# Kernel tuning notes

Hardware: AMD Instinct MI355X
Metric: run time of the kernel (lower is better)

## Reference

```python
import jax, jax.numpy as jnp
import numpy as np

N_VARS = 2048
D_GRAPH = 256
NUM_ADJ = 7
ALPHA = 0.9
MASK = 0.5


def setup_inputs() -> dict:
    key = jax.random.key(0)
    ks = jax.random.split(key, 8)
    init_adj = jax.random.uniform(ks[0], (N_VARS, N_VARS), dtype=jnp.float32, minval=-1.0, maxval=1.0)
    emb1 = jax.random.normal(ks[1], (NUM_ADJ, N_VARS, D_GRAPH), dtype=jnp.float32)
    emb2 = jax.random.normal(ks[2], (NUM_ADJ, N_VARS, D_GRAPH), dtype=jnp.float32)
    lim = 1.0 / np.sqrt(D_GRAPH)
    w1 = jax.random.uniform(ks[3], (NUM_ADJ, D_GRAPH, D_GRAPH), dtype=jnp.float32, minval=-lim, maxval=lim)
    b1 = jax.random.uniform(ks[4], (NUM_ADJ, D_GRAPH), dtype=jnp.float32, minval=-lim, maxval=lim)
    w2 = jax.random.uniform(ks[5], (NUM_ADJ, D_GRAPH, D_GRAPH), dtype=jnp.float32, minval=-lim, maxval=lim)
    b2 = jax.random.uniform(ks[6], (NUM_ADJ, D_GRAPH), dtype=jnp.float32, minval=-lim, maxval=lim)
    time_indices = jax.random.randint(ks[7], (8,), 0, NUM_ADJ)
    return {
        'init_adj': init_adj, 'emb1': emb1, 'emb2': emb2,
        'w1': w1, 'b1': b1, 'w2': w2, 'b2': b2,
        'time_indices': time_indices, 'current_epoch': 10,
    }


def reference(init_adj, emb1, emb2, w1, b1, w2, b2, time_indices, current_epoch):
    n = init_adj.shape[0]
    k = int(n * n * MASK)
    prop = min(current_epoch / 5, ALPHA)  # static python scalar schedule
    eye = jnp.eye(n, dtype=init_adj.dtype)

    def build_one(e1, e2, W1, B1, W2, B2):
        # nn.Linear: x @ W.T + b, then tanh
        nv1 = jnp.tanh(e1 @ W1.T + B1)          # [n, d]
        nv2 = jnp.tanh(e2 @ W2.T + B2)          # [n, d]
        a = (1.0 - prop) * init_adj + prop * (nv1 @ nv2.T)  # [n, n]
        adj = jax.nn.relu(jnp.tanh(a))
        adj = adj * (1.0 - eye)                 # remove diagonal
        flat = adj.reshape(-1)
        _, idx = jax.lax.top_k(flat, k)         # data-dependent sparsification
        m = jnp.zeros_like(flat).at[idx].set(1.0)
        adj = m.reshape(n, n) * adj
        adj = adj + eye
        return adj / adj.sum(axis=1, keepdims=True)  # row-degree normalize

    oadj = jax.vmap(build_one)(emb1, emb2, w1, b1, w2, b2)  # [num_adj, n, n]
    return oadj[time_indices]  # [B, n, n]
```

## Files before the change

kernel.cpp:

```cpp
#include <hip/hip_runtime.h>
#include <cstdint>
#include <cstddef>

#define NVARS 2048
#define DG    256
#define NSLOT 8
#define NN2   (NVARS*NVARS)
#define K_SEL 2097152u
#define CAP   (1u<<18)
#define KS    512

typedef __attribute__((ext_vector_type(8))) short short8;
typedef __attribute__((ext_vector_type(8))) unsigned short ushort8;
typedef __attribute__((ext_vector_type(4))) float floatx4;

__device__ __align__(16) unsigned short g_ebig[NSLOT][2][NVARS*KS];
__device__ __align__(16) unsigned short g_wbig[NSLOT][2][DG*KS];
__device__ __align__(16) unsigned short g_abig[NSLOT][NVARS*KS];
__device__ __align__(16) unsigned short g_bbig[NSLOT][NVARS*KS];
__device__ unsigned g_hist[NSLOT][2048];
__device__ unsigned g_cand[NSLOT][CAP];
__device__ unsigned g_state[NSLOT][16];
__device__ float g_scal[2];

__device__ __forceinline__ unsigned fkey(float x){
  unsigned b = __float_as_uint(x);
  return (b & 0x80000000u) ? ~b : (b | 0x80000000u);
}
__device__ __forceinline__ unsigned short f2bf(float v){
  unsigned u = __float_as_uint(v);
  return (unsigned short)((u + 0x7FFFu + ((u >> 16) & 1u)) >> 16);
}
__device__ __forceinline__ void async16(void* lds, const void* g){
  __builtin_amdgcn_global_load_lds(
      (const __attribute__((address_space(1))) unsigned int*)g,
      (__attribute__((address_space(3))) unsigned int*)lds, 16, 0, 0);
}

__global__ __launch_bounds__(256) void k_prep(const int* __restrict__ tind,
                                              const int* __restrict__ epoch_p){
  int tid = threadIdx.x;
  if (tid < NSLOT){
    int t = tind[tid];
    int fo = tid;
    for (int b = 0; b < tid; b++){ if (tind[b] == t){ fo = b; break; } }
    g_state[tid][0] = (fo == tid) ? 1u : 0u;
    g_state[tid][1] = (unsigned)fo;
    g_state[tid][2] = 0u;
    g_state[tid][3] = K_SEL;
    g_state[tid][4] = 0u;
    g_state[tid][7] = 0x7FFFFFFFu;
    g_state[tid][8] = 0u;
  }
  if (tid == 0){
    double pd = (double)epoch_p[0] / 5.0;
    if (pd > 0.9) pd = 0.9;
    g_scal[0] = (float)(1.0 - pd);
    g_scal[1] = (float)pd;
  }
  unsigned* h = (unsigned*)g_hist;
  for (int i = tid; i < NSLOT*2048; i += 256) h[i] = 0u;
}

__global__ __launch_bounds__(256) void k_split(
    const float* __restrict__ emb1, const float* __restrict__ emb2,
    const float* __restrict__ w1,  const float* __restrict__ w2,
    const int* __restrict__ tind){
  int z = blockIdx.z; int s = z >> 1; int side = z & 1;
  if (!g_state[s][0]) return;
  int t = tind[s];
  int flat = blockIdx.x*256 + threadIdx.x;
  const float* src;
  unsigned short* dst;
  if (flat < 65536){
    int row = flat >> 5, g8 = flat & 31;
    src = (side ? emb2 : emb1) + (size_t)t*NVARS*DG + (size_t)row*DG + g8*8;
    dst = g_ebig[s][side] + (size_t)row*KS + g8*8;
  } else {
    int f2 = flat - 65536;
    int row = f2 >> 5, g8 = f2 & 31;
    src = (side ? w2 : w1) + (size_t)t*DG*DG + (size_t)row*DG + g8*8;
    dst = g_wbig[s][side] + (size_t)row*KS + g8*8;
  }
  float4 v0 = *(const float4*)src;
  float4 v1 = *(const float4*)(src + 4);
  float a[8] = {v0.x,v0.y,v0.z,v0.w,v1.x,v1.y,v1.z,v1.w};
  ushort8 hi8, lo8;
  #pragma unroll
  for (int j = 0; j < 8; j++){
    unsigned short hb = f2bf(a[j]);
    float hv = __uint_as_float(((unsigned)hb) << 16);
    hi8[j] = hb;
    lo8[j] = f2bf(a[j] - hv);
  }
  *(ushort8*)dst         = hi8;
  *(ushort8*)(dst + 256) = lo8;
}

__global__ __launch_bounds__(256, 2) void k_gemm_nv(
    const float* __restrict__ b1, const float* __restrict__ b2,
    const int* __restrict__ tind){
  int z = blockIdx.z; int s = z >> 1; int side = z & 1;
  if (!g_state[s][0]) return;
  int t = tind[s];
  const unsigned short* __restrict__ A = g_ebig[s][side];
  const unsigned short* __restrict__ B = g_wbig[s][side];
  const float* __restrict__ bias = (side ? b2 : b1) + (size_t)t*DG;
  unsigned short* __restrict__ dst = side ? g_bbig[s] : g_abig[s];
  __shared__ __align__(16) unsigned short As[128*64];
  __shared__ __align__(16) unsigned short Bs[128*64];
  __shared__ __align__(16) float Cs[128][68];
  int tid = threadIdx.x;
  int lane = tid & 63, wv = tid >> 6;
  int rowBase = blockIdx.y*128, colBase = blockIdx.x*128;
  int rW = (wv >> 1)*64, cW = (wv & 1)*64;
  int m = lane & 15, q = lane >> 4;
  int rl = lane >> 3, sl = lane & 7;
  floatx4 acc[4][4] = {};
  for (int p = 0; p < 3; p++){
    int aoff = (p == 1) ? 256 : 0;
    int boff = (p == 2) ? 256 : 0;
    for (int k0 = 0; k0 < 256; k0 += 64){
      #pragma unroll
      for (int t4 = 0; t4 < 4; t4++){
        int rloc = wv*32 + t4*8 + rl;
        int g = sl ^ (rloc & 7);
        async16(&As[(wv*32 + t4*8)*64], A + (size_t)(rowBase + rloc)*KS + aoff + k0 + g*8);
        async16(&Bs[(wv*32 + t4*8)*64], B + (size_t)(colBase + rloc)*KS + boff + k0 + g*8);
      }
      __syncthreads();
      #pragma unroll
      for (int kk = 0; kk < 2; kk++){
        short8 af[4], bfr[4];
        #pragma unroll
        for (int i = 0; i < 4; i++){
          int rA = rW + i*16 + m;
          af[i]  = *(const short8*)&As[rA*64 + (((kk*4 + q) ^ (rA & 7))*8)];
          int rB = cW + i*16 + m;
          bfr[i] = *(const short8*)&Bs[rB*64 + (((kk*4 + q) ^ (rB & 7))*8)];
        }
        #pragma unroll
        for (int i = 0; i < 4; i++)
          #pragma unroll
          for (int j = 0; j < 4; j++)
            acc[i][j] = __builtin_amdgcn_mfma_f32_16x16x32_bf16(af[i], bfr[j], acc[i][j], 0, 0, 0);
      }
      __syncthreads();
    }
  }
  for (int h = 0; h < 2; h++){
    if ((wv & 1) == h){
      #pragma unroll
      for (int i = 0; i < 4; i++)
        #pragma unroll
        for (int j = 0; j < 4; j++)
          #pragma unroll
          for (int r = 0; r < 4; r++)
            Cs[rW + i*16 + q*4 + r][j*16 + m] = acc[i][j][r];
    }
    __syncthreads();
    #pragma unroll
    for (int it = 0; it < 4; it++){
      int row = it*32 + (tid >> 3);
      int c8  = (tid & 7)*8;
      float4 va = *(const float4*)&Cs[row][c8];
      float4 vb = *(const float4*)&Cs[row][c8 + 4];
      float v[8] = {va.x,va.y,va.z,va.w,vb.x,vb.y,vb.z,vb.w};
      int colb = colBase + h*64 + c8;
      ushort8 hi8, lo8;
      #pragma unroll
      for (int j = 0; j < 8; j++){
        float e = tanhf(v[j] + bias[colb + j]);
        unsigned short hb = f2bf(e);
        float hv = __uint_as_float(((unsigned)hb) << 16);
        hi8[j] = hb;
        lo8[j] = f2bf(e - hv);
      }
      unsigned short* rp = dst + (size_t)(rowBase + row)*KS;
      *(ushort8*)(rp + colb)       = hi8;
      *(ushort8*)(rp + 256 + colb) = lo8;
    }
    __syncthreads();
  }
}

__global__ __launch_bounds__(256, 2) void k_gemm_s(const float* __restrict__ init,
                                                   float* __restrict__ out){
  int s = blockIdx.z;
  if (!g_state[s][0]) return;
  const unsigned short* __restrict__ A = g_abig[s];
  const unsigned short* __restrict__ B = g_bbig[s];
  __shared__ __align__(16) unsigned short As[128*64];
  __shared__ __align__(16) unsigned short Bs[128*64];
  int tid = threadIdx.x;
  int lane = tid & 63, wv = tid >> 6;
  int rowBase = blockIdx.y*128, colBase = blockIdx.x*128;
  int rW = (wv >> 1)*64, cW = (wv & 1)*64;
  int m = lane & 15, q = lane >> 4;
  int rl = lane >> 3, sl = lane & 7;
  floatx4 acc[4][4] = {};
  for (int p = 0; p < 3; p++){
    int aoff = (p == 1) ? 256 : 0;
    int boff = (p == 2) ? 256 : 0;
    for (int k0 = 0; k0 < 256; k0 += 64){
      #pragma unroll
      for (int t4 = 0; t4 < 4; t4++){
        int rloc = wv*32 + t4*8 + rl;
        int g = sl ^ (rloc & 7);
        async16(&As[(wv*32 + t4*8)*64], A + (size_t)(rowBase + rloc)*KS + aoff + k0 + g*8);
        async16(&Bs[(wv*32 + t4*8)*64], B + (size_t)(colBase + rloc)*KS + boff + k0 + g*8);
      }
      __syncthreads();
      #pragma unroll
      for (int kk = 0; kk < 2; kk++){
        short8 af[4], bfr[4];
        #pragma unroll
        for (int i = 0; i < 4; i++){
          int rA = rW + i*16 + m;
          af[i]  = *(const short8*)&As[rA*64 + (((kk*4 + q) ^ (rA & 7))*8)];
          int rB = cW + i*16 + m;
          bfr[i] = *(const short8*)&Bs[rB*64 + (((kk*4 + q) ^ (rB & 7))*8)];
        }
        #pragma unroll
        for (int i = 0; i < 4; i++)
          #pragma unroll
          for (int j = 0; j < 4; j++)
            acc[i][j] = __builtin_amdgcn_mfma_f32_16x16x32_bf16(af[i], bfr[j], acc[i][j], 0, 0, 0);
      }
      __syncthreads();
    }
  }
  float am1 = g_scal[0], am2 = g_scal[1];
  float* __restrict__ outs = out + (size_t)s*NN2;
  #pragma unroll
  for (int i = 0; i < 4; i++){
    #pragma unroll
    for (int j = 0; j < 4; j++){
      int col = colBase + cW + j*16 + m;
      #pragma unroll
      for (int r = 0; r < 4; r++){
        int row = rowBase + rW + i*16 + q*4 + r;
        float val = am1*init[(size_t)row*NVARS + col] + am2*acc[i][j][r];
        if (row == col) val = -__builtin_inff();
        outs[(size_t)row*NVARS + col] = val;
      }
    }
  }
}

__global__ __launch_bounds__(256) void k_hist1(const float* __restrict__ out){
  int s = blockIdx.z;
  if (!g_state[s][0]) return;
  __shared__ unsigned h[2048];
  int tid = threadIdx.x;
  for (int i = tid; i < 2048; i += 256) h[i] = 0u;
  __syncthreads();
  const float4* p = (const float4*)(out + (size_t)s*NN2);
  int stride = gridDim.x*256;
  for (int i = blockIdx.x*256 + tid; i < NN2/4; i += stride){
    float4 v = p[i];
    float xs[4] = {v.x, v.y, v.z, v.w};
    #pragma unroll
    for (int j = 0; j < 4; j++) atomicAdd(&h[fkey(xs[j]) >> 21], 1u);
  }
  __syncthreads();
  for (int i = tid; i < 2048; i += 256){
    unsigned c = h[i];
    if (c) atomicAdd(&g_hist[s][i], c);
  }
}

__device__ void desc_select(unsigned* h, unsigned* sc, int nb, unsigned rank,
                            unsigned* od, unsigned* orem, unsigned* ocnt){
  int tid = threadIdx.x;
  int per = nb >> 8;
  unsigned loc[8];
  unsigned own = 0;
  int base = tid*per;
  for (int j = 0; j < per; j++){ loc[j] = h[base+j]; own += loc[j]; }
  sc[tid] = own;
  __syncthreads();
  for (int off = 1; off < 256; off <<= 1){
    unsigned v = (tid + off < 256) ? sc[tid+off] : 0u;
    __syncthreads();
    sc[tid] += v;
    __syncthreads();
  }
  unsigned acc = sc[tid] - own;
  for (int j = per-1; j >= 0; j--){
    unsigned c = loc[j];
    if (c && rank > acc && rank <= acc + c){ *od = (unsigned)(base+j); *orem = rank - acc; *ocnt = c; }
    acc += c;
  }
  __syncthreads();
}
__device__ void asc_select(unsigned* h, unsigned* sc, int nb, unsigned rank,
                           unsigned* od, unsigned* orem){
  int tid = threadIdx.x;
  int per = nb >> 8;
  unsigned loc[8];
  unsigned own = 0;
  int base = tid*per;
  for (int j = 0; j < per; j++){ loc[j] = h[base+j]; own += loc[j]; }
  sc[tid] = own;
  __syncthreads();
  for (int off = 1; off < 256; off <<= 1){
    unsigned v = (tid >= off) ? sc[tid-off] : 0u;
    __syncthreads();
    sc[tid] += v;
    __syncthreads();
  }
  unsigned below = sc[tid] - own;
  for (int j = 0; j < per; j++){
    unsigned c = loc[j];
    if (c && rank > below && rank <= below + c){ *od = (unsigned)(base+j); *orem = rank - below; }
    below += c;
  }
  __syncthreads();
}

__global__ __launch_bounds__(256) void k_select1(){
  int s = blockIdx.x;
  if (!g_state[s][0]) return;
  int tid = threadIdx.x;
  __shared__ unsigned h[2048];
  __shared__ unsigned sc[256];
  __shared__ unsigned sd, srem, scnt;
  for (int i = tid; i < 2048; i += 256) h[i] = g_hist[s][i];
  if (tid == 0){ sd = 0; srem = 1; scnt = 1; }
  __syncthreads();
  desc_select(h, sc, 2048, K_SEL, &sd, &srem, &scnt);
  if (tid == 0){ g_state[s][2] = sd << 21; g_state[s][3] = srem; }
}

__global__ __launch_bounds__(256) void k_collect(const float* __restrict__ out){
  int s = blockIdx.z;
  if (!g_state[s][0]) return;
  unsigned pb = g_state[s][2] >> 21;
  const float4* p = (const float4*)(out + (size_t)s*NN2);
  int stride = gridDim.x*256;
  for (int i = blockIdx.x*256 + threadIdx.x; i < NN2/4; i += stride){
    float4 v = p[i];
    float xs[4] = {v.x, v.y, v.z, v.w};
    #pragma unroll
    for (int j = 0; j < 4; j++){
      if ((fkey(xs[j]) >> 21) == pb){
        unsigned pos = atomicAdd(&g_state[s][8], 1u);
        if (pos < CAP) g_cand[s][pos] = (unsigned)(i*4 + j);
      }
    }
  }
}

__global__ __launch_bounds__(256) void k_final(const float* __restrict__ out){
  int s = blockIdx.x;
  if (!g_state[s][0]) return;
  int tid = threadIdx.x;
  unsigned mcnt = g_state[s][8]; if (mcnt > CAP) mcnt = CAP;
  unsigned krem = g_state[s][3];
  unsigned prefix = g_state[s][2];
  const float* outs = out + (size_t)s*NN2;
  __shared__ unsigned h[2048];
  __shared__ unsigned sc[256];
  __shared__ unsigned sd, srem, scnt;
  for (int i = tid; i < 2048; i += 256) h[i] = 0u;
  if (tid == 0){ sd = 0; srem = 1; scnt = 1; }
  __syncthreads();
  for (unsigned i = tid; i < mcnt; i += 256){
    unsigned u = fkey(outs[g_cand[s][i]]);
    atomicAdd(&h[(u >> 10) & 0x7FFu], 1u);
  }
  __syncthreads();
  desc_select(h, sc, 2048, krem, &sd, &srem, &scnt);
  unsigned d1 = sd, krem2 = srem;
  __syncthreads();
  for (int i = tid; i < 2048; i += 256) h[i] = 0u;
  __syncthreads();
  for (unsigned i = tid; i < mcnt; i += 256){
    unsigned u = fkey(outs[g_cand[s][i]]);
    if (((u >> 10) & 0x7FFu) == d1) atomicAdd(&h[u & 0x3FFu], 1u);
  }
  __syncthreads();
  desc_select(h, sc, 1024, krem2, &sd, &srem, &scnt);
  unsigned d0 = sd, nek = srem, cnteq = scnt;
  __syncthreads();
  unsigned tu = prefix | (d1 << 10) | d0;
  unsigned cutoff = 0x7FFFFFFFu;
  if (nek < cnteq){
    for (int i = tid; i < 2048; i += 256) h[i] = 0u;
    __syncthreads();
    for (unsigned i = tid; i < mcnt; i += 256){
      unsigned idx = g_cand[s][i];
      if (fkey(outs[idx]) == tu) atomicAdd(&h[idx >> 11], 1u);
    }
    __syncthreads();
    asc_select(h, sc, 2048, nek, &sd, &srem);
    unsigned dh = sd, j2 = srem;
    __syncthreads();
    for (int i = tid; i < 2048; i += 256) h[i] = 0u;
    __syncthreads();
    for (unsigned i = tid; i < mcnt; i += 256){
      unsigned idx = g_cand[s][i];
      if (fkey(outs[idx]) == tu && (idx >> 11) == dh) atomicAdd(&h[idx & 0x7FFu], 1u);
    }
    __syncthreads();
    asc_select(h, sc, 2048, j2, &sd, &srem);
    cutoff = (dh << 11) | sd;
    __syncthreads();
  }
  if (tid == 0){ g_state[s][4] = tu; g_state[s][7] = cutoff; }
}

__global__ __launch_bounds__(256) void k_masknorm(float* __restrict__ out){
  int s = blockIdx.y;
  if (!g_state[s][0]) return;
  int r = blockIdx.x;
  int tid = threadIdx.x;
  unsigned tu = g_state[s][4];
  unsigned cutoff = g_state[s][7];
  const float4* rowp = (const float4*)(out + (size_t)s*NN2 + (size_t)r*NVARS);
  unsigned baseIdx = (unsigned)(r*NVARS);
  float4 res[2];
  double lsum = 0.0;
  #pragma unroll
  for (int t = 0; t < 2; t++){
    int c4 = tid + t*256;
    float4 a4 = rowp[c4];
    float av[4] = {a4.x, a4.y, a4.z, a4.w};
    float rv[4];
    #pragma unroll
    for (int j = 0; j < 4; j++){
      int c = c4*4 + j;
      float vv;
      if (c == r) vv = 1.0f;
      else {
        unsigned u = fkey(av[j]);
        bool keep = (u > tu) || (u == tu && (baseIdx + (unsigned)c) <= cutoff);
        vv = keep ? fmaxf(tanhf(av[j]), 0.0f) : 0.0f;
      }
      rv[j] = vv;
      lsum += (double)vv;
    }
    res[t].x = rv[0]; res[t].y = rv[1]; res[t].z = rv[2]; res[t].w = rv[3];
  }
  __shared__ double red[256];
  red[tid] = lsum;
  __syncthreads();
  for (int off = 128; off > 0; off >>= 1){
    if (tid < off) red[tid] += red[tid+off];
    __syncthreads();
  }
  float inv = 1.0f / (float)red[0];
  #pragma unroll
  for (int t = 0; t < 2; t++){
    res[t].x *= inv; res[t].y *= inv; res[t].z *= inv; res[t].w *= inv;
  }
  for (int s2 = 0; s2 < NSLOT; s2++){
    if (g_state[s2][1] == (unsigned)s){
      float4* dst = (float4*)(out + (size_t)s2*NN2 + (size_t)r*NVARS);
      dst[tid]       = res[0];
      dst[tid + 256] = res[1];
    }
  }
}

extern "C" void kernel_launch(void* const* d_in, const int* in_sizes, int n_in,
                              void* d_out, int out_size, void* d_ws, size_t ws_size,
                              hipStream_t stream){
  (void)in_sizes; (void)n_in; (void)d_ws; (void)ws_size; (void)out_size;
  const float* init = (const float*)d_in[0];
  const float* emb1 = (const float*)d_in[1];
  const float* emb2 = (const float*)d_in[2];
  const float* w1   = (const float*)d_in[3];
  const float* b1   = (const float*)d_in[4];
  const float* w2   = (const float*)d_in[5];
  const float* b2   = (const float*)d_in[6];
  const int* tind   = (const int*)d_in[7];
  const int* epoch  = (const int*)d_in[8];
  float* out = (float*)d_out;

  k_prep<<<1, 256, 0, stream>>>(tind, epoch);
  k_split<<<dim3(288, 1, 16), 256, 0, stream>>>(emb1, emb2, w1, w2, tind);
  k_gemm_nv<<<dim3(2, 16, 16), 256, 0, stream>>>(b1, b2, tind);
  k_gemm_s<<<dim3(16, 16, 8), 256, 0, stream>>>(init, out);
  k_hist1<<<dim3(256, 1, 8), 256, 0, stream>>>(out);
  k_select1<<<8, 256, 0, stream>>>();
  k_collect<<<dim3(256, 1, 8), 256, 0, stream>>>(out);
  k_final<<<8, 256, 0, stream>>>(out);
  k_masknorm<<<dim3(2048, 8), 256, 0, stream>>>(out);
}
```

Baseline: 364.8 us.

## Drop prep kernel, widen similarity GEMM tile, replicate histogram bins

Removes the k_prep launch. Each kernel now works out the first occurrence of its time index inline, and the selection kernels reset the histogram and counters for the next call. The similarity GEMM tile grows to 256x128, so each wave handles 64 rows across all 128 columns, which improves reuse of the B tile and halves the number of blocks. The coarse histogram pass spreads LDS atomics over four replicated histograms to cut contention. The risks are higher register pressure from 128 accumulators per thread and correctness that depends on state left clean by the previous call.

```diff
diff --git a/kernel.cpp b/kernel.cpp
--- a/kernel.cpp
+++ b/kernel.cpp
@@ -21,7 +21,6 @@
 __device__ unsigned g_hist[NSLOT][2048];
 __device__ unsigned g_cand[NSLOT][CAP];
 __device__ unsigned g_state[NSLOT][16];
-__device__ float g_scal[2];
 
 __device__ __forceinline__ unsigned fkey(float x){
   unsigned b = __float_as_uint(x);
@@ -36,30 +35,10 @@
       (const __attribute__((address_space(1))) unsigned int*)g,
       (__attribute__((address_space(3))) unsigned int*)lds, 16, 0, 0);
 }
-
-__global__ __launch_bounds__(256) void k_prep(const int* __restrict__ tind,
-                                              const int* __restrict__ epoch_p){
-  int tid = threadIdx.x;
-  if (tid < NSLOT){
-    int t = tind[tid];
-    int fo = tid;
-    for (int b = 0; b < tid; b++){ if (tind[b] == t){ fo = b; break; } }
-    g_state[tid][0] = (fo == tid) ? 1u : 0u;
-    g_state[tid][1] = (unsigned)fo;
-    g_state[tid][2] = 0u;
-    g_state[tid][3] = K_SEL;
-    g_state[tid][4] = 0u;
-    g_state[tid][7] = 0x7FFFFFFFu;
-    g_state[tid][8] = 0u;
-  }
-  if (tid == 0){
-    double pd = (double)epoch_p[0] / 5.0;
-    if (pd > 0.9) pd = 0.9;
-    g_scal[0] = (float)(1.0 - pd);
-    g_scal[1] = (float)pd;
-  }
-  unsigned* h = (unsigned*)g_hist;
-  for (int i = tid; i < NSLOT*2048; i += 256) h[i] = 0u;
+__device__ __forceinline__ int first_occ(const int* __restrict__ tind, int s){
+  int t = tind[s]; int f = s;
+  for (int b = s - 1; b >= 0; b--) if (tind[b] == t) f = b;
+  return f;
 }
 
 __global__ __launch_bounds__(256) void k_split(
@@ -67,7 +46,7 @@
     const float* __restrict__ w1,  const float* __restrict__ w2,
     const int* __restrict__ tind){
   int z = blockIdx.z; int s = z >> 1; int side = z & 1;
-  if (!g_state[s][0]) return;
+  if (first_occ(tind, s) != s) return;
   int t = tind[s];
   int flat = blockIdx.x*256 + threadIdx.x;
   const float* src;
@@ -101,7 +80,7 @@
     const float* __restrict__ b1, const float* __restrict__ b2,
     const int* __restrict__ tind){
   int z = blockIdx.z; int s = z >> 1; int side = z & 1;
-  if (!g_state[s][0]) return;
+  if (first_occ(tind, s) != s) return;
   int t = tind[s];
   const unsigned short* __restrict__ A = g_ebig[s][side];
   const unsigned short* __restrict__ B = g_wbig[s][side];
@@ -185,61 +164,73 @@
 }
 
 __global__ __launch_bounds__(256, 2) void k_gemm_s(const float* __restrict__ init,
-                                                   float* __restrict__ out){
+                                                   float* __restrict__ out,
+                                                   const int* __restrict__ tind,
+                                                   const int* __restrict__ epoch_p){
   int s = blockIdx.z;
-  if (!g_state[s][0]) return;
+  if (first_occ(tind, s) != s) return;
+  double pd = (double)epoch_p[0] / 5.0;
+  if (pd > 0.9) pd = 0.9;
+  float am1 = (float)(1.0 - pd);
+  float am2 = (float)pd;
   const unsigned short* __restrict__ A = g_abig[s];
   const unsigned short* __restrict__ B = g_bbig[s];
-  __shared__ __align__(16) unsigned short As[128*64];
+  __shared__ __align__(16) unsigned short As[256*64];
   __shared__ __align__(16) unsigned short Bs[128*64];
   int tid = threadIdx.x;
   int lane = tid & 63, wv = tid >> 6;
-  int rowBase = blockIdx.y*128, colBase = blockIdx.x*128;
-  int rW = (wv >> 1)*64, cW = (wv & 1)*64;
+  int rowBase = blockIdx.y*256, colBase = blockIdx.x*128;
   int m = lane & 15, q = lane >> 4;
   int rl = lane >> 3, sl = lane & 7;
-  floatx4 acc[4][4] = {};
+  floatx4 acc[4][8] = {};
   for (int p = 0; p < 3; p++){
     int aoff = (p == 1) ? 256 : 0;
     int boff = (p == 2) ? 256 : 0;
     for (int k0 = 0; k0 < 256; k0 += 64){
       #pragma unroll
-      for (int t4 = 0; t4 < 4; t4++){
-        int rloc = wv*32 + t4*8 + rl;
+      for (int it = 0; it < 8; it++){
+        int rloc = it*32 + wv*8 + rl;
         int g = sl ^ (rloc & 7);
-        async16(&As[(wv*32 + t4*8)*64], A + (size_t)(rowBase + rloc)*KS + aoff + k0 + g*8);
-        async16(&Bs[(wv*32 + t4*8)*64], B + (size_t)(colBase + rloc)*KS + boff + k0 + g*8);
+        async16(&As[(it*32 + wv*8)*64], A + (size_t)(rowBase + rloc)*KS + aoff + k0 + g*8);
+      }
+      #pragma unroll
+      for (int it = 0; it < 4; it++){
+        int rloc = it*32 + wv*8 + rl;
+        int g = sl ^ (rloc & 7);
+        async16(&Bs[(it*32 + wv*8)*64], B + (size_t)(colBase + rloc)*KS + boff + k0 + g*8);
       }
       __syncthreads();
       #pragma unroll
       for (int kk = 0; kk < 2; kk++){
-        short8 af[4], bfr[4];
+        short8 af[4], bfr[8];
         #pragma unroll
         for (int i = 0; i < 4; i++){
-          int rA = rW + i*16 + m;
-          af[i]  = *(const short8*)&As[rA*64 + (((kk*4 + q) ^ (rA & 7))*8)];
-          int rB = cW + i*16 + m;
-          bfr[i] = *(const short8*)&Bs[rB*64 + (((kk*4 + q) ^ (rB & 7))*8)];
+          int rA = wv*64 + i*16 + m;
+          af[i] = *(const short8*)&As[rA*64 + (((kk*4 + q) ^ (rA & 7))*8)];
+        }
+        #pragma unroll
+        for (int j = 0; j < 8; j++){
+          int rB = j*16 + m;
+          bfr[j] = *(const short8*)&Bs[rB*64 + (((kk*4 + q) ^ (rB & 7))*8)];
         }
         #pragma unroll
         for (int i = 0; i < 4; i++)
           #pragma unroll
-          for (int j = 0; j < 4; j++)
+          for (int j = 0; j < 8; j++)
             acc[i][j] = __builtin_amdgcn_mfma_f32_16x16x32_bf16(af[i], bfr[j], acc[i][j], 0, 0, 0);
       }
       __syncthreads();
     }
   }
-  float am1 = g_scal[0], am2 = g_scal[1];
   float* __restrict__ outs = out + (size_t)s*NN2;
   #pragma unroll
   for (int i = 0; i < 4; i++){
     #pragma unroll
-    for (int j = 0; j < 4; j++){
-      int col = colBase + cW + j*16 + m;
+    for (int j = 0; j < 8; j++){
+      int col = colBase + j*16 + m;
       #pragma unroll
       for (int r = 0; r < 4; r++){
-        int row = rowBase + rW + i*16 + q*4 + r;
+        int row = rowBase + wv*64 + i*16 + q*4 + r;
         float val = am1*init[(size_t)row*NVARS + col] + am2*acc[i][j][r];
         if (row == col) val = -__builtin_inff();
         outs[(size_t)row*NVARS + col] = val;
@@ -248,24 +239,26 @@
   }
 }
 
-__global__ __launch_bounds__(256) void k_hist1(const float* __restrict__ out){
+__global__ __launch_bounds__(256) void k_hist1(const float* __restrict__ out,
+                                               const int* __restrict__ tind){
   int s = blockIdx.z;
-  if (!g_state[s][0]) return;
-  __shared__ unsigned h[2048];
-  int tid = threadIdx.x;
-  for (int i = tid; i < 2048; i += 256) h[i] = 0u;
-  __syncthreads();
+  if (first_occ(tind, s) != s) return;
+  __shared__ unsigned h[4*2049];
+  int tid = threadIdx.x;
+  for (int i = tid; i < 4*2049; i += 256) h[i] = 0u;
+  __syncthreads();
+  unsigned rep = (unsigned)(tid & 3) * 2049u;
   const float4* p = (const float4*)(out + (size_t)s*NN2);
   int stride = gridDim.x*256;
   for (int i = blockIdx.x*256 + tid; i < NN2/4; i += stride){
     float4 v = p[i];
     float xs[4] = {v.x, v.y, v.z, v.w};
     #pragma unroll
-    for (int j = 0; j < 4; j++) atomicAdd(&h[fkey(xs[j]) >> 21], 1u);
+    for (int j = 0; j < 4; j++) atomicAdd(&h[rep + (fkey(xs[j]) >> 21)], 1u);
   }
   __syncthreads();
   for (int i = tid; i < 2048; i += 256){
-    unsigned c = h[i];
+    unsigned c = h[i] + h[2049 + i] + h[2*2049 + i] + h[3*2049 + i];
     if (c) atomicAdd(&g_hist[s][i], c);
   }
 }
@@ -319,9 +312,9 @@
   __syncthreads();
 }
 
-__global__ __launch_bounds__(256) void k_select1(){
+__global__ __launch_bounds__(256) void k_select1(const int* __restrict__ tind){
   int s = blockIdx.x;
-  if (!g_state[s][0]) return;
+  if (first_occ(tind, s) != s) return;
   int tid = threadIdx.x;
   __shared__ unsigned h[2048];
   __shared__ unsigned sc[256];
@@ -331,11 +324,13 @@
   __syncthreads();
   desc_select(h, sc, 2048, K_SEL, &sd, &srem, &scnt);
   if (tid == 0){ g_state[s][2] = sd << 21; g_state[s][3] = srem; }
-}
-
-__global__ __launch_bounds__(256) void k_collect(const float* __restrict__ out){
+  for (int i = tid; i < 2048; i += 256) g_hist[s][i] = 0u;
+}
+
+__global__ __launch_bounds__(256) void k_collect(const float* __restrict__ out,
+                                                 const int* __restrict__ tind){
   int s = blockIdx.z;
-  if (!g_state[s][0]) return;
+  if (first_occ(tind, s) != s) return;
   unsigned pb = g_state[s][2] >> 21;
   const float4* p = (const float4*)(out + (size_t)s*NN2);
   int stride = gridDim.x*256;
@@ -352,9 +347,10 @@
   }
 }
 
-__global__ __launch_bounds__(256) void k_final(const float* __restrict__ out){
+__global__ __launch_bounds__(256) void k_final(const float* __restrict__ out,
+                                               const int* __restrict__ tind){
   int s = blockIdx.x;
-  if (!g_state[s][0]) return;
+  if (first_occ(tind, s) != s) return;
   int tid = threadIdx.x;
   unsigned mcnt = g_state[s][8]; if (mcnt > CAP) mcnt = CAP;
   unsigned krem = g_state[s][3];
@@ -408,12 +404,17 @@
     cutoff = (dh << 11) | sd;
     __syncthreads();
   }
-  if (tid == 0){ g_state[s][4] = tu; g_state[s][7] = cutoff; }
-}
-
-__global__ __launch_bounds__(256) void k_masknorm(float* __restrict__ out){
+  if (tid == 0){
+    g_state[s][4] = tu;
+    g_state[s][7] = cutoff;
+    g_state[s][8] = 0u;
+  }
+}
+
+__global__ __launch_bounds__(256) void k_masknorm(float* __restrict__ out,
+                                                  const int* __restrict__ tind){
   int s = blockIdx.y;
-  if (!g_state[s][0]) return;
+  if (first_occ(tind, s) != s) return;
   int r = blockIdx.x;
   int tid = threadIdx.x;
   unsigned tu = g_state[s][4];
@@ -456,7 +457,7 @@
     res[t].x *= inv; res[t].y *= inv; res[t].z *= inv; res[t].w *= inv;
   }
   for (int s2 = 0; s2 < NSLOT; s2++){
-    if (g_state[s2][1] == (unsigned)s){
+    if (first_occ(tind, s2) == s){
       float4* dst = (float4*)(out + (size_t)s2*NN2 + (size_t)r*NVARS);
       dst[tid]       = res[0];
       dst[tid + 256] = res[1];
@@ -479,13 +480,12 @@
   const int* epoch  = (const int*)d_in[8];
   float* out = (float*)d_out;
 
-  k_prep<<<1, 256, 0, stream>>>(tind, epoch);
   k_split<<<dim3(288, 1, 16), 256, 0, stream>>>(emb1, emb2, w1, w2, tind);
   k_gemm_nv<<<dim3(2, 16, 16), 256, 0, stream>>>(b1, b2, tind);
-  k_gemm_s<<<dim3(16, 16, 8), 256, 0, stream>>>(init, out);
-  k_hist1<<<dim3(256, 1, 8), 256, 0, stream>>>(out);
-  k_select1<<<8, 256, 0, stream>>>();
-  k_collect<<<dim3(256, 1, 8), 256, 0, stream>>>(out);
-  k_final<<<8, 256, 0, stream>>>(out);
-  k_masknorm<<<dim3(2048, 8), 256, 0, stream>>>(out);
-}
+  k_gemm_s<<<dim3(16, 8, 8), 256, 0, stream>>>(init, out, tind, epoch);
+  k_hist1<<<dim3(256, 1, 8), 256, 0, stream>>>(out, tind);
+  k_select1<<<8, 256, 0, stream>>>(tind);
+  k_collect<<<dim3(256, 1, 8), 256, 0, stream>>>(out, tind);
+  k_final<<<8, 256, 0, stream>>>(out, tind);
+  k_masknorm<<<dim3(2048, 8), 256, 0, stream>>>(out, tind);
+}
```

Measured after the change: 380.8 us. +4.4%, slower.
